# Performance work log

Hardware: AMD Instinct MI355X
Metric: run time of the kernel (lower is better)

## Reference

```python
import jax, jax.numpy as jnp
import numpy as np

L, B, S, D, H = 4, 4, 2048, 512, 8
DH = D // H
FF = 4 * D
BN_EPS = 1e-3  # keras BatchNormalization default epsilon


def setup_inputs() -> dict:
    key = jax.random.key(0)
    ks = jax.random.split(key, 8)
    g = lambda k, shape: jax.random.normal(k, shape, dtype=jnp.float32) * 0.02
    return {
        "sequence": jax.random.normal(ks[0], (B, S, D), dtype=jnp.float32),
        "wq": g(ks[1], (L, D, D)), "bq": jnp.zeros((L, D), jnp.float32),
        "wk": g(ks[2], (L, D, D)), "bk": jnp.zeros((L, D), jnp.float32),
        "wv": g(ks[3], (L, D, D)), "bv": jnp.zeros((L, D), jnp.float32),
        "wo": g(ks[4], (L, D, D)), "bo": jnp.zeros((L, D), jnp.float32),
        "w1": g(ks[5], (L, D, FF)), "b1": jnp.zeros((L, FF), jnp.float32),
        "w2": g(ks[6], (L, FF, D)), "b2": jnp.zeros((L, D), jnp.float32),
        "g1": jnp.ones((L, D), jnp.float32), "be1": jnp.zeros((L, D), jnp.float32),
        "g2": jnp.ones((L, D), jnp.float32), "be2": jnp.zeros((L, D), jnp.float32),
    }


def reference(sequence, wq, bq, wk, bk, wv, bv, wo, bo, w1, b1, w2, b2, g1, be1, g2, be2):
    # Inference-mode BatchNorm with moving_mean=0, moving_var=1:
    # bn(x) = x / sqrt(1 + eps) * gamma + beta
    bn_inv = 1.0 / jnp.sqrt(jnp.float32(1.0 + BN_EPS))
    scale = 1.0 / jnp.sqrt(jnp.float32(DH))
    x = sequence  # [B, S, D]
    for i in range(L):
        # Batched multi-head self-attention (== the per-position loop concat)
        q = (x @ wq[i] + bq[i]).reshape(B, S, H, DH)
        k = (x @ wk[i] + bk[i]).reshape(B, S, H, DH)
        v = (x @ wv[i] + bv[i]).reshape(B, S, H, DH)
        att = jax.nn.softmax(jnp.einsum('bqhd,bkhd->bhqk', q, k) * scale, axis=-1)
        o = jnp.einsum('bhqk,bkhd->bqhd', att, v).reshape(B, S, D)
        o = o @ wo[i] + bo[i]
        x = (x + o) * bn_inv * g1[i] + be1[i]          # residual + BN
        f = jax.nn.relu(x @ w1[i] + b1[i]) @ w2[i] + b2[i]  # FFN
        x = (x + f) * bn_inv * g2[i] + be2[i]          # residual + BN
    return x
```

## Files before the change

kernel.cpp:

```cpp
#include <hip/hip_runtime.h>
#include <hip/hip_bf16.h>

#define BB   4
#define SS   2048
#define DDIM 512
#define HH   8
#define DHD  64
#define FFD  2048
#define LLN  4
#define NQKV 1536
#define BN_INV 0.9995003747f
#define QSCALE 0.18033688011112042f

typedef __bf16 bf16x8 __attribute__((ext_vector_type(8)));
typedef __bf16 bf16x4 __attribute__((ext_vector_type(4)));
typedef float  f32x4  __attribute__((ext_vector_type(4)));
typedef float  f32x16 __attribute__((ext_vector_type(16)));

__device__ __forceinline__ void gl2lds16(const void* g, void* l) {
  __builtin_amdgcn_global_load_lds((const __attribute__((address_space(1))) void*)g,
                                   (__attribute__((address_space(3))) void*)l, 16, 0, 0);
}

__device__ __forceinline__ unsigned pkbf16(float a, float b) {
  union { __bf16 h[2]; unsigned u; } x;
  x.h[0] = (__bf16)a; x.h[1] = (__bf16)b;
  return x.u;
}

__global__ __launch_bounds__(256) void k_transpose_w(const float* __restrict__ in,
                                                     __bf16* __restrict__ out,
                                                     int R, int C,
                                                     size_t in_zs, size_t out_zs) {
  __shared__ float tile[32][33];
  in += (size_t)blockIdx.z * in_zs;
  out += (size_t)blockIdx.z * out_zs;
  const int c0 = blockIdx.x * 32, r0 = blockIdx.y * 32;
  const int tx = threadIdx.x & 31, ty = threadIdx.x >> 5;
#pragma unroll
  for (int k = 0; k < 4; ++k) {
    int r = ty + k * 8;
    tile[r][tx] = in[(size_t)(r0 + r) * C + (c0 + tx)];
  }
  __syncthreads();
#pragma unroll
  for (int k = 0; k < 4; ++k) {
    int c = ty + k * 8;
    out[(size_t)(c0 + c) * R + (r0 + tx)] = (__bf16)tile[tx][c];
  }
}

__global__ __launch_bounds__(256) void k_bias_fuse(const float* __restrict__ bq,
                                                   const float* __restrict__ bk,
                                                   const float* __restrict__ bv,
                                                   float* __restrict__ out) {
  const int i = blockIdx.x * 256 + threadIdx.x;
  const int l = i / NQKV, j = i - l * NQKV;
  float v = (j < 512) ? bq[l * 512 + j]
          : (j < 1024) ? bk[l * 512 + j - 512]
                       : bv[l * 512 + j - 1024];
  out[i] = v;
}

__global__ __launch_bounds__(256) void k_transpose_v(const __bf16* __restrict__ qkv,
                                                     __bf16* __restrict__ vt) {
  __shared__ __bf16 tile[32][33];
  const int s0 = blockIdx.x * 32;
  const int d0 = blockIdx.y * 32;
  const int bh = blockIdx.z, b = bh >> 3, h = bh & 7;
  const int tx = threadIdx.x & 31, ty = threadIdx.x >> 5;
#pragma unroll
  for (int k = 0; k < 4; ++k) {
    int s = ty + k * 8;
    tile[s][tx] = qkv[(size_t)(b * SS + s0 + s) * NQKV + 2 * DDIM + h * DHD + d0 + tx];
  }
  __syncthreads();
#pragma unroll
  for (int k = 0; k < 4; ++k) {
    int d = ty + k * 8;
    vt[(size_t)(bh * DHD + d0 + d) * SS + (s0 + tx)] = tile[tx][d];
  }
}

__global__ __launch_bounds__(256) void k_cast(const float* __restrict__ in,
                                              float* __restrict__ xf,
                                              __bf16* __restrict__ xb) {
  const int i = (blockIdx.x * 256 + threadIdx.x) * 4;
  const float4 v = *(const float4*)(in + i);
  *(float4*)(xf + i) = v;
  bf16x4 o;
  o[0] = (__bf16)v.x; o[1] = (__bf16)v.y; o[2] = (__bf16)v.z; o[3] = (__bf16)v.w;
  *(bf16x4*)(xb + i) = o;
}

template <int EPI>
__global__ __launch_bounds__(256) void k_gemm_bt(const __bf16* __restrict__ A,
                                                 const __bf16* __restrict__ Bt,
                                                 const float* __restrict__ bias,
                                                 __bf16* __restrict__ Cb,
                                                 int M, int N, int K,
                                                 const float* __restrict__ xres,
                                                 float* __restrict__ xout,
                                                 const float* __restrict__ gvec,
                                                 const float* __restrict__ bvec) {
  __shared__ char As[2][16384];
  __shared__ char Bs[2][16384];
  const int tid = threadIdx.x;
  const int l = tid & 63, w = tid >> 6;
  const int wm = w >> 1, wn = w & 1;
  const int m0 = blockIdx.y * 128, n0 = blockIdx.x * 128;
  const int lr = l & 15, lg = l >> 4;
  f32x4 acc[4][4] = {};
  const int nk = K >> 6;
  const size_t ldab = (size_t)K * 2;

  auto stage = [&](int buf, int kt) {
    const int k0b = kt * 128;
#pragma unroll
    for (int i = 0; i < 4; ++i) {
      const int chunk = i * 256 + tid;
      const int row = chunk >> 3;
      const int scb = ((chunk & 7) * 16) ^ ((row & 7) << 4);
      gl2lds16((const char*)A + (size_t)(m0 + row) * ldab + k0b + scb,
               As[buf] + (i * 256 + w * 64) * 16);
      gl2lds16((const char*)Bt + (size_t)(n0 + row) * ldab + k0b + scb,
               Bs[buf] + (i * 256 + w * 64) * 16);
    }
  };

  stage(0, 0);
  __syncthreads();
  int cur = 0;
  for (int kt = 0; kt < nk; ++kt) {
    if (kt + 1 < nk) stage(cur ^ 1, kt + 1);
#pragma unroll
    for (int kk = 0; kk < 2; ++kk) {
      bf16x8 a[4], b[4];
#pragma unroll
      for (int m = 0; m < 4; ++m) {
        const int row = wm * 64 + m * 16 + lr;
        const int cb = kk * 64 + lg * 16;
        a[m] = *(const bf16x8*)(As[cur] + row * 128 + (cb ^ ((row & 7) << 4)));
      }
#pragma unroll
      for (int n = 0; n < 4; ++n) {
        const int row = wn * 64 + n * 16 + lr;
        const int cb = kk * 64 + lg * 16;
        b[n] = *(const bf16x8*)(Bs[cur] + row * 128 + (cb ^ ((row & 7) << 4)));
      }
#pragma unroll
      for (int m = 0; m < 4; ++m)
#pragma unroll
        for (int n = 0; n < 4; ++n)
          acc[m][n] = __builtin_amdgcn_mfma_f32_16x16x32_bf16(a[m], b[n], acc[m][n], 0, 0, 0);
    }
    asm volatile("s_waitcnt vmcnt(0)" ::: "memory");
    __syncthreads();
    cur ^= 1;
  }
#pragma unroll
  for (int m = 0; m < 4; ++m) {
    const int gm = m0 + wm * 64 + m * 16 + lg * 4;
#pragma unroll
    for (int n = 0; n < 4; ++n) {
      const int gn = n0 + wn * 64 + n * 16 + lr;
      const float bv_ = bias[gn];
#pragma unroll
      for (int j = 0; j < 4; ++j) {
        const size_t idx = (size_t)(gm + j) * N + gn;
        float v = acc[m][n][j] + bv_;
        if constexpr (EPI == 1) {
          Cb[idx] = (__bf16)fmaxf(v, 0.0f);
        } else if constexpr (EPI == 2) {
          float t = (xres[idx] + v) * BN_INV * gvec[gn] + bvec[gn];
          xout[idx] = t;
          Cb[idx] = (__bf16)t;
        } else {
          if (gn < DDIM) v *= QSCALE;
          Cb[idx] = (__bf16)v;
        }
      }
    }
  }
}

__global__ __launch_bounds__(256, 2) void k_attn(const __bf16* __restrict__ QKV,
                                                 const __bf16* __restrict__ Vt,
                                                 __bf16* __restrict__ O) {
  __shared__ char smem[65536];
  const int tid = threadIdx.x, l = tid & 63, w = tid >> 6;
  const int lq = l & 31, hi = l >> 5;
  const int f = blockIdx.y * 16 + blockIdx.x;
  const int L = (f & 7) * 64 + (f >> 3);
  const int qt = L & 15, bh = L >> 4;
  const int b = bh >> 3, h = bh & 7;
  const int myq = qt * 128 + w * 32 + lq;
  bf16x8 qf[4];
  {
    const __bf16* qp = QKV + (size_t)(b * SS + myq) * NQKV + h * DHD + hi * 8;
#pragma unroll
    for (int kc = 0; kc < 4; ++kc)
      qf[kc] = *(const bf16x8*)(qp + kc * 16);
  }
  f32x16 oaccT[2] = {};
  float rsum = 0.f;

  auto stage = [&](int buf, int t) {
    const int kv0 = t * 128;
    char* Kd = smem + buf * 16384;
    char* Vd = smem + 32768 + buf * 16384;
#pragma unroll
    for (int i = 0; i < 4; ++i) {
      const int chunk = i * 256 + tid;
      const int row = chunk >> 3;
      const int rs = row ^ ((((row >> 2) + 1) & 2) * 6);
      const int scb = ((chunk & 7) * 16) ^ ((row & 7) << 4);
      gl2lds16((const char*)QKV + ((size_t)(b * SS + kv0 + rs) * NQKV + DDIM + h * DHD) * 2 + scb,
               Kd + (i * 256 + w * 64) * 16);
    }
#pragma unroll
    for (int i = 0; i < 4; ++i) {
      const int chunk = i * 256 + tid;
      const int row = chunk >> 4;
      const int scb = ((chunk & 15) * 16) ^ ((row & 15) << 4);
      gl2lds16((const char*)Vt + ((size_t)(bh * DHD + row) * SS + kv0) * 2 + scb,
               Vd + (i * 256 + w * 64) * 16);
    }
  };

  stage(0, 0);
  __syncthreads();
  int cur = 0;
  for (int t = 0; t < SS / 128; ++t) {
    if (t < SS / 128 - 1) stage(cur ^ 1, t + 1);
    const char* Ks = smem + cur * 16384;
    const char* Vs = smem + 32768 + cur * 16384;
#pragma unroll
    for (int kt2 = 0; kt2 < 4; ++kt2) {
      const int krow = kt2 * 32 + lq;
      const int kswz = (krow & 7) << 4;
      f32x16 st = {};
      __builtin_amdgcn_s_setprio(1);
#pragma unroll
      for (int kc = 0; kc < 4; ++kc) {
        bf16x8 kf = *(const bf16x8*)(Ks + krow * 128 + ((kc * 32 + hi * 16) ^ kswz));
        st = __builtin_amdgcn_mfma_f32_32x32x16_bf16(kf, qf[kc], st, 0, 0, 0);
      }
      __builtin_amdgcn_s_setprio(0);
      unsigned pk8[8];
#pragma unroll
      for (int i = 0; i < 8; ++i) {
        const float e0 = __builtin_amdgcn_exp2f(st[2 * i]);
        const float e1 = __builtin_amdgcn_exp2f(st[2 * i + 1]);
        rsum += e0 + e1;
        pk8[i] = pkbf16(e0, e1);
      }
      union { unsigned u[4]; bf16x8 v; } pf0, pf1;
#pragma unroll
      for (int i = 0; i < 4; ++i) { pf0.u[i] = pk8[i]; pf1.u[i] = pk8[4 + i]; }
      __builtin_amdgcn_s_setprio(1);
#pragma unroll
      for (int dt = 0; dt < 2; ++dt) {
        const int vrow = dt * 32 + lq;
        const int vswz = (vrow & 15) << 4;
        bf16x8 vf0 = *(const bf16x8*)(Vs + vrow * 256 + ((kt2 * 64 + hi * 16) ^ vswz));
        bf16x8 vf1 = *(const bf16x8*)(Vs + vrow * 256 + ((kt2 * 64 + 32 + hi * 16) ^ vswz));
        oaccT[dt] = __builtin_amdgcn_mfma_f32_32x32x16_bf16(vf0, pf0.v, oaccT[dt], 0, 0, 0);
        oaccT[dt] = __builtin_amdgcn_mfma_f32_32x32x16_bf16(vf1, pf1.v, oaccT[dt], 0, 0, 0);
      }
      __builtin_amdgcn_s_setprio(0);
    }
    asm volatile("s_waitcnt vmcnt(0)" ::: "memory");
    __syncthreads();
    cur ^= 1;
  }
  rsum += __shfl_xor(rsum, 32);
  const float inv = 1.0f / rsum;
  __bf16* op = O + (size_t)(b * SS + myq) * DDIM + h * DHD;
#pragma unroll
  for (int dt = 0; dt < 2; ++dt)
#pragma unroll
    for (int g = 0; g < 4; ++g) {
      const int d0 = dt * 32 + g * 8 + hi * 4;
      unsigned u0 = pkbf16(oaccT[dt][4 * g + 0] * inv, oaccT[dt][4 * g + 1] * inv);
      unsigned u1 = pkbf16(oaccT[dt][4 * g + 2] * inv, oaccT[dt][4 * g + 3] * inv);
      uint2 uu; uu.x = u0; uu.y = u1;
      *(uint2*)(op + d0) = uu;
    }
}

static constexpr size_t SZ_WQKVT = (size_t)LLN * NQKV * DDIM * 2;
static constexpr size_t SZ_WOT   = (size_t)LLN * DDIM * DDIM * 2;
static constexpr size_t SZ_WT_DF = (size_t)LLN * DDIM * FFD * 2;
static constexpr size_t SZ_BQKV  = (size_t)LLN * NQKV * 4;
static constexpr size_t SZ_X     = (size_t)BB * SS * DDIM * 4;
static constexpr size_t SZ_ABF   = (size_t)BB * SS * DDIM * 2;
static constexpr size_t SZ_QKV   = (size_t)BB * SS * NQKV * 2;
static constexpr size_t OFF_WQKVT = 0;
static constexpr size_t OFF_WOT  = OFF_WQKVT + SZ_WQKVT;
static constexpr size_t OFF_W1T  = OFF_WOT + SZ_WOT;
static constexpr size_t OFF_W2T  = OFF_W1T + SZ_WT_DF;
static constexpr size_t OFF_BQKV = OFF_W2T + SZ_WT_DF;
static constexpr size_t OFF_X    = OFF_BQKV + SZ_BQKV;
static constexpr size_t OFF_XB   = OFF_X + SZ_X;
static constexpr size_t OFF_QKV  = OFF_XB + SZ_ABF;
static constexpr size_t OFF_VT   = OFF_QKV + SZ_QKV;
static constexpr size_t OFF_OB   = OFF_VT + SZ_ABF;
static constexpr size_t OFF_H1   = OFF_QKV;

extern "C" void kernel_launch(void* const* d_in, const int* in_sizes, int n_in,
                              void* d_out, int out_size, void* d_ws, size_t ws_size,
                              hipStream_t stream) {
  const float* seq = (const float*)d_in[0];
  const float* wq = (const float*)d_in[1];  const float* bq = (const float*)d_in[2];
  const float* wk = (const float*)d_in[3];  const float* bk = (const float*)d_in[4];
  const float* wv = (const float*)d_in[5];  const float* bv = (const float*)d_in[6];
  const float* wo = (const float*)d_in[7];  const float* bo = (const float*)d_in[8];
  const float* w1 = (const float*)d_in[9];  const float* b1 = (const float*)d_in[10];
  const float* w2 = (const float*)d_in[11]; const float* b2 = (const float*)d_in[12];
  const float* g1 = (const float*)d_in[13]; const float* be1 = (const float*)d_in[14];
  const float* g2 = (const float*)d_in[15]; const float* be2 = (const float*)d_in[16];

  char* ws = (char*)d_ws;
  __bf16* wqkvt = (__bf16*)(ws + OFF_WQKVT);
  __bf16* wot = (__bf16*)(ws + OFF_WOT);
  __bf16* w1t = (__bf16*)(ws + OFF_W1T);
  __bf16* w2t = (__bf16*)(ws + OFF_W2T);
  float*  bqkv = (float*)(ws + OFF_BQKV);
  float*  xf  = (float*)(ws + OFF_X);
  __bf16* xb  = (__bf16*)(ws + OFF_XB);
  __bf16* qkvb = (__bf16*)(ws + OFF_QKV);
  __bf16* vtb = (__bf16*)(ws + OFF_VT);
  __bf16* ob  = (__bf16*)(ws + OFF_OB);
  __bf16* h1  = (__bf16*)(ws + OFF_H1);

  const size_t zDD = (size_t)DDIM * DDIM;
  const size_t zQKV = (size_t)NQKV * DDIM;
  const size_t zDF = (size_t)DDIM * FFD;
  k_transpose_w<<<dim3(16, 16, LLN), 256, 0, stream>>>(wq, wqkvt, DDIM, DDIM, zDD, zQKV);
  k_transpose_w<<<dim3(16, 16, LLN), 256, 0, stream>>>(wk, wqkvt + (size_t)DDIM * DDIM, DDIM, DDIM, zDD, zQKV);
  k_transpose_w<<<dim3(16, 16, LLN), 256, 0, stream>>>(wv, wqkvt + (size_t)2 * DDIM * DDIM, DDIM, DDIM, zDD, zQKV);
  k_transpose_w<<<dim3(16, 16, LLN), 256, 0, stream>>>(wo, wot, DDIM, DDIM, zDD, zDD);
  k_transpose_w<<<dim3(64, 16, LLN), 256, 0, stream>>>(w1, w1t, DDIM, FFD, zDF, zDF);
  k_transpose_w<<<dim3(16, 64, LLN), 256, 0, stream>>>(w2, w2t, FFD, DDIM, zDF, zDF);
  k_bias_fuse<<<LLN * NQKV / 256, 256, 0, stream>>>(bq, bk, bv, bqkv);
  k_cast<<<4096, 256, 0, stream>>>(seq, xf, xb);

  const int M = BB * SS;
  for (int i = 0; i < LLN; ++i) {
    k_gemm_bt<3><<<dim3(NQKV / 128, M / 128), 256, 0, stream>>>(
        xb, wqkvt + (size_t)i * NQKV * DDIM, bqkv + i * NQKV, qkvb, M, NQKV, DDIM,
        nullptr, nullptr, nullptr, nullptr);
    k_transpose_v<<<dim3(SS / 32, DHD / 32, BB * HH), 256, 0, stream>>>(qkvb, vtb);
    k_attn<<<dim3(SS / 128, BB * HH), 256, 0, stream>>>(qkvb, vtb, ob);
    k_gemm_bt<2><<<dim3(DDIM / 128, M / 128), 256, 0, stream>>>(
        ob, wot + (size_t)i * DDIM * DDIM, bo + i * DDIM, xb, M, DDIM, DDIM,
        xf, xf, g1 + i * DDIM, be1 + i * DDIM);
    k_gemm_bt<1><<<dim3(FFD / 128, M / 128), 256, 0, stream>>>(
        xb, w1t + (size_t)i * DDIM * FFD, b1 + i * FFD, h1, M, FFD, DDIM,
        nullptr, nullptr, nullptr, nullptr);
    k_gemm_bt<2><<<dim3(DDIM / 128, M / 128), 256, 0, stream>>>(
        h1, w2t + (size_t)i * DDIM * FFD, b2 + i * DDIM, xb, M, DDIM, FFD,
        xf, (i == LLN - 1) ? (float*)d_out : xf, g2 + i * DDIM, be2 + i * DDIM);
  }
  (void)in_sizes; (void)n_in; (void)out_size; (void)ws_size;
}
```

Before: 642.5 us.

## Add 256x256-tile 8-wave GEMM with interleaved prefetch for QKV and FFN1

Adds a new GEMM kernel that uses 256x256 output tiles and 512 threads (8 waves, each computing 128x64). It splits the per-k-tile work into four MFMA phases, with LDS fragment loads and the next tile's global-to-LDS prefetch interleaved between them, and raises wave priority around the MFMA blocks. The QKV projection and the first FFN GEMM now use this kernel to increase data reuse per block and overlap loads with compute. The trade-off is fewer blocks (grids of 6x32 and 8x32), 128KB of LDS per block giving one block per CU, and more barriers per k-step.

```diff
diff --git a/kernel.cpp b/kernel.cpp
--- a/kernel.cpp
+++ b/kernel.cpp
@@ -28,6 +28,8 @@
   return x.u;
 }
 
+#define SBAR() do { __builtin_amdgcn_s_barrier(); asm volatile("" ::: "memory"); } while (0)
+
 __global__ __launch_bounds__(256) void k_transpose_w(const float* __restrict__ in,
                                                      __bf16* __restrict__ out,
                                                      int R, int C,
@@ -103,8 +105,8 @@
                                                  float* __restrict__ xout,
                                                  const float* __restrict__ gvec,
                                                  const float* __restrict__ bvec) {
-  __shared__ char As[2][16384];
-  __shared__ char Bs[2][16384];
+  __shared__ __align__(16) char As[2][16384];
+  __shared__ __align__(16) char Bs[2][16384];
   const int tid = threadIdx.x;
   const int l = tid & 63, w = tid >> 6;
   const int wm = w >> 1, wn = w & 1;
@@ -175,6 +177,159 @@
           float t = (xres[idx] + v) * BN_INV * gvec[gn] + bvec[gn];
           xout[idx] = t;
           Cb[idx] = (__bf16)t;
+        } else {
+          if (gn < DDIM) v *= QSCALE;
+          Cb[idx] = (__bf16)v;
+        }
+      }
+    }
+  }
+}
+
+template <int EPI>
+__global__ __launch_bounds__(512, 1) void k_gemm256(const __bf16* __restrict__ A,
+                                                    const __bf16* __restrict__ Bt,
+                                                    const float* __restrict__ bias,
+                                                    __bf16* __restrict__ Cb,
+                                                    int M, int N, int K) {
+  __shared__ __align__(16) char As[2][32768];
+  __shared__ __align__(16) char Bs[2][32768];
+  const int tid = threadIdx.x;
+  const int l = tid & 63, w = tid >> 6;
+  const int wm = w >> 2, wn = w & 3;
+  const int m0 = blockIdx.y * 256, n0 = blockIdx.x * 256;
+  const int lr = l & 15, lg = l >> 4;
+  f32x4 acc[8][4] = {};
+  const int nk = K >> 6;
+  const size_t ldab = (size_t)K * 2;
+
+  auto stA = [&](int buf, int kt, int h) {
+    const int k0b = kt * 128;
+#pragma unroll
+    for (int i = 0; i < 2; ++i) {
+      const int chunk = h * 1024 + i * 512 + tid;
+      const int row = chunk >> 3;
+      const int scb = ((chunk & 7) * 16) ^ ((row & 7) << 4);
+      gl2lds16((const char*)A + (size_t)(m0 + row) * ldab + k0b + scb,
+               As[buf] + (h * 1024 + i * 512 + w * 64) * 16);
+    }
+  };
+  auto stB = [&](int buf, int kt, int h) {
+    const int k0b = kt * 128;
+#pragma unroll
+    for (int i = 0; i < 2; ++i) {
+      const int chunk = h * 1024 + i * 512 + tid;
+      const int row = chunk >> 3;
+      const int scb = ((chunk & 7) * 16) ^ ((row & 7) << 4);
+      gl2lds16((const char*)Bt + (size_t)(n0 + row) * ldab + k0b + scb,
+               Bs[buf] + (h * 1024 + i * 512 + w * 64) * 16);
+    }
+  };
+
+  stA(0, 0, 0); stA(0, 0, 1); stB(0, 0, 0); stB(0, 0, 1);
+  asm volatile("s_waitcnt vmcnt(0)" ::: "memory");
+  SBAR();
+
+  int cur = 0;
+  for (int kt = 0; kt < nk; ++kt) {
+    const char* Ac = As[cur];
+    const char* Bc = Bs[cur];
+    const int oth = cur ^ 1;
+    const bool pf = (kt + 1 < nk);
+    bf16x8 af[4][2], bfr[4][2];
+#pragma unroll
+    for (int mi = 0; mi < 4; ++mi) {
+      const int row = wm * 128 + mi * 16 + lr;
+      const int swz = (row & 7) << 4;
+#pragma unroll
+      for (int kk = 0; kk < 2; ++kk)
+        af[mi][kk] = *(const bf16x8*)(Ac + row * 128 + ((kk * 64 + lg * 16) ^ swz));
+    }
+#pragma unroll
+    for (int ni = 0; ni < 2; ++ni) {
+      const int row = wn * 64 + ni * 16 + lr;
+      const int swz = (row & 7) << 4;
+#pragma unroll
+      for (int kk = 0; kk < 2; ++kk)
+        bfr[ni][kk] = *(const bf16x8*)(Bc + row * 128 + ((kk * 64 + lg * 16) ^ swz));
+    }
+    if (pf) { stA(oth, kt + 1, 0); stA(oth, kt + 1, 1); }
+    SBAR();
+    __builtin_amdgcn_s_setprio(1);
+#pragma unroll
+    for (int mi = 0; mi < 4; ++mi)
+#pragma unroll
+      for (int ni = 0; ni < 2; ++ni)
+#pragma unroll
+        for (int kk = 0; kk < 2; ++kk)
+          acc[mi][ni] = __builtin_amdgcn_mfma_f32_16x16x32_bf16(af[mi][kk], bfr[ni][kk], acc[mi][ni], 0, 0, 0);
+    __builtin_amdgcn_s_setprio(0);
+    SBAR();
+#pragma unroll
+    for (int ni = 2; ni < 4; ++ni) {
+      const int row = wn * 64 + ni * 16 + lr;
+      const int swz = (row & 7) << 4;
+#pragma unroll
+      for (int kk = 0; kk < 2; ++kk)
+        bfr[ni][kk] = *(const bf16x8*)(Bc + row * 128 + ((kk * 64 + lg * 16) ^ swz));
+    }
+    if (pf) { stB(oth, kt + 1, 0); stB(oth, kt + 1, 1); }
+    SBAR();
+    __builtin_amdgcn_s_setprio(1);
+#pragma unroll
+    for (int mi = 0; mi < 4; ++mi)
+#pragma unroll
+      for (int ni = 2; ni < 4; ++ni)
+#pragma unroll
+        for (int kk = 0; kk < 2; ++kk)
+          acc[mi][ni] = __builtin_amdgcn_mfma_f32_16x16x32_bf16(af[mi][kk], bfr[ni][kk], acc[mi][ni], 0, 0, 0);
+    __builtin_amdgcn_s_setprio(0);
+    SBAR();
+#pragma unroll
+    for (int mi = 0; mi < 4; ++mi) {
+      const int row = wm * 128 + (mi + 4) * 16 + lr;
+      const int swz = (row & 7) << 4;
+#pragma unroll
+      for (int kk = 0; kk < 2; ++kk)
+        af[mi][kk] = *(const bf16x8*)(Ac + row * 128 + ((kk * 64 + lg * 16) ^ swz));
+    }
+    SBAR();
+    __builtin_amdgcn_s_setprio(1);
+#pragma unroll
+    for (int mi = 0; mi < 4; ++mi)
+#pragma unroll
+      for (int ni = 0; ni < 2; ++ni)
+#pragma unroll
+        for (int kk = 0; kk < 2; ++kk)
+          acc[mi + 4][ni] = __builtin_amdgcn_mfma_f32_16x16x32_bf16(af[mi][kk], bfr[ni][kk], acc[mi + 4][ni], 0, 0, 0);
+    __builtin_amdgcn_s_setprio(0);
+    SBAR();
+    __builtin_amdgcn_s_setprio(1);
+#pragma unroll
+    for (int mi = 0; mi < 4; ++mi)
+#pragma unroll
+      for (int ni = 2; ni < 4; ++ni)
+#pragma unroll
+        for (int kk = 0; kk < 2; ++kk)
+          acc[mi + 4][ni] = __builtin_amdgcn_mfma_f32_16x16x32_bf16(af[mi][kk], bfr[ni][kk], acc[mi + 4][ni], 0, 0, 0);
+    __builtin_amdgcn_s_setprio(0);
+    asm volatile("s_waitcnt vmcnt(0)" ::: "memory");
+    SBAR();
+    cur ^= 1;
+  }
+#pragma unroll
+  for (int mi = 0; mi < 8; ++mi) {
+    const int gm = m0 + wm * 128 + mi * 16 + lg * 4;
+#pragma unroll
+    for (int ni = 0; ni < 4; ++ni) {
+      const int gn = n0 + wn * 64 + ni * 16 + lr;
+      const float bv_ = bias[gn];
+#pragma unroll
+      for (int j = 0; j < 4; ++j) {
+        const size_t idx = (size_t)(gm + j) * N + gn;
+        float v = acc[mi][ni][j] + bv_;
+        if constexpr (EPI == 1) {
+          Cb[idx] = (__bf16)fmaxf(v, 0.0f);
         } else {
           if (gn < DDIM) v *= QSCALE;
           Cb[idx] = (__bf16)v;
@@ -348,17 +503,15 @@
 
   const int M = BB * SS;
   for (int i = 0; i < LLN; ++i) {
-    k_gemm_bt<3><<<dim3(NQKV / 128, M / 128), 256, 0, stream>>>(
-        xb, wqkvt + (size_t)i * NQKV * DDIM, bqkv + i * NQKV, qkvb, M, NQKV, DDIM,
-        nullptr, nullptr, nullptr, nullptr);
+    k_gemm256<3><<<dim3(NQKV / 256, M / 256), 512, 0, stream>>>(
+        xb, wqkvt + (size_t)i * NQKV * DDIM, bqkv + i * NQKV, qkvb, M, NQKV, DDIM);
     k_transpose_v<<<dim3(SS / 32, DHD / 32, BB * HH), 256, 0, stream>>>(qkvb, vtb);
     k_attn<<<dim3(SS / 128, BB * HH), 256, 0, stream>>>(qkvb, vtb, ob);
     k_gemm_bt<2><<<dim3(DDIM / 128, M / 128), 256, 0, stream>>>(
         ob, wot + (size_t)i * DDIM * DDIM, bo + i * DDIM, xb, M, DDIM, DDIM,
         xf, xf, g1 + i * DDIM, be1 + i * DDIM);
-    k_gemm_bt<1><<<dim3(FFD / 128, M / 128), 256, 0, stream>>>(
-        xb, w1t + (size_t)i * DDIM * FFD, b1 + i * FFD, h1, M, FFD, DDIM,
-        nullptr, nullptr, nullptr, nullptr);
+    k_gemm256<1><<<dim3(FFD / 256, M / 256), 512, 0, stream>>>(
+        xb, w1t + (size_t)i * DDIM * FFD, b1 + i * FFD, h1, M, FFD, DDIM);
     k_gemm_bt<2><<<dim3(DDIM / 128, M / 128), 256, 0, stream>>>(
         h1, w2t + (size_t)i * DDIM * FFD, b2 + i * DDIM, xb, M, DDIM, FFD,
         xf, (i == LLN - 1) ? (float*)d_out : xf, g2 + i * DDIM, be2 + i * DDIM);
```

New measurement: 641.4 us. Within noise of the previous version (-0.2%).

## Use triple-buffered 512-thread GEMM with partial vmcnt waits and MFMA priority

Applied to the files above, without the earlier changes.

Replaces the double-buffered 256-thread GEMM with a 512-thread version on the same 128x128 tile. Each wave now computes 64x32, and shared-memory staging is triple-buffered, so loads run two k-steps ahead. Each step waits on vmcnt(4) instead of draining all loads and uses one barrier per iteration. s_setprio is raised around the MFMA block. The aim is to hide global-load latency better and to give each CU more waves, at the cost of 96KB of LDS per block (one block per CU) and fewer accumulators per wave.

```diff
diff --git a/kernel.cpp b/kernel.cpp
--- a/kernel.cpp
+++ b/kernel.cpp
@@ -28,6 +28,8 @@
   return x.u;
 }
 
+#define SBAR() do { __builtin_amdgcn_s_barrier(); asm volatile("" ::: "memory"); } while (0)
+
 __global__ __launch_bounds__(256) void k_transpose_w(const float* __restrict__ in,
                                                      __bf16* __restrict__ out,
                                                      int R, int C,
@@ -94,81 +96,95 @@
 }
 
 template <int EPI>
-__global__ __launch_bounds__(256) void k_gemm_bt(const __bf16* __restrict__ A,
-                                                 const __bf16* __restrict__ Bt,
-                                                 const float* __restrict__ bias,
-                                                 __bf16* __restrict__ Cb,
-                                                 int M, int N, int K,
-                                                 const float* __restrict__ xres,
-                                                 float* __restrict__ xout,
-                                                 const float* __restrict__ gvec,
-                                                 const float* __restrict__ bvec) {
-  __shared__ char As[2][16384];
-  __shared__ char Bs[2][16384];
+__global__ __launch_bounds__(512, 1) void k_gemm3(const __bf16* __restrict__ A,
+                                                  const __bf16* __restrict__ Bt,
+                                                  const float* __restrict__ bias,
+                                                  __bf16* __restrict__ Cb,
+                                                  int M, int N, int K,
+                                                  const float* __restrict__ xres,
+                                                  float* __restrict__ xout,
+                                                  const float* __restrict__ gvec,
+                                                  const float* __restrict__ bvec) {
+  __shared__ __align__(16) char As[3][16384];
+  __shared__ __align__(16) char Bs[3][16384];
   const int tid = threadIdx.x;
   const int l = tid & 63, w = tid >> 6;
-  const int wm = w >> 1, wn = w & 1;
+  const int wm = w >> 2, wn = w & 3;
   const int m0 = blockIdx.y * 128, n0 = blockIdx.x * 128;
   const int lr = l & 15, lg = l >> 4;
-  f32x4 acc[4][4] = {};
+  f32x4 acc[4][2] = {};
   const int nk = K >> 6;
   const size_t ldab = (size_t)K * 2;
 
   auto stage = [&](int buf, int kt) {
     const int k0b = kt * 128;
 #pragma unroll
-    for (int i = 0; i < 4; ++i) {
-      const int chunk = i * 256 + tid;
+    for (int i = 0; i < 2; ++i) {
+      const int chunk = i * 512 + tid;
       const int row = chunk >> 3;
       const int scb = ((chunk & 7) * 16) ^ ((row & 7) << 4);
       gl2lds16((const char*)A + (size_t)(m0 + row) * ldab + k0b + scb,
-               As[buf] + (i * 256 + w * 64) * 16);
+               As[buf] + (i * 512 + w * 64) * 16);
       gl2lds16((const char*)Bt + (size_t)(n0 + row) * ldab + k0b + scb,
-               Bs[buf] + (i * 256 + w * 64) * 16);
+               Bs[buf] + (i * 512 + w * 64) * 16);
     }
   };
 
   stage(0, 0);
-  __syncthreads();
-  int cur = 0;
+  stage(1, 1);
+  int bc = 0;
   for (int kt = 0; kt < nk; ++kt) {
-    if (kt + 1 < nk) stage(cur ^ 1, kt + 1);
-#pragma unroll
-    for (int kk = 0; kk < 2; ++kk) {
-      bf16x8 a[4], b[4];
-#pragma unroll
-      for (int m = 0; m < 4; ++m) {
-        const int row = wm * 64 + m * 16 + lr;
-        const int cb = kk * 64 + lg * 16;
-        a[m] = *(const bf16x8*)(As[cur] + row * 128 + (cb ^ ((row & 7) << 4)));
-      }
-#pragma unroll
-      for (int n = 0; n < 4; ++n) {
-        const int row = wn * 64 + n * 16 + lr;
-        const int cb = kk * 64 + lg * 16;
-        b[n] = *(const bf16x8*)(Bs[cur] + row * 128 + (cb ^ ((row & 7) << 4)));
-      }
-#pragma unroll
-      for (int m = 0; m < 4; ++m)
-#pragma unroll
-        for (int n = 0; n < 4; ++n)
-          acc[m][n] = __builtin_amdgcn_mfma_f32_16x16x32_bf16(a[m], b[n], acc[m][n], 0, 0, 0);
-    }
-    asm volatile("s_waitcnt vmcnt(0)" ::: "memory");
-    __syncthreads();
-    cur ^= 1;
-  }
-#pragma unroll
-  for (int m = 0; m < 4; ++m) {
-    const int gm = m0 + wm * 64 + m * 16 + lg * 4;
-#pragma unroll
-    for (int n = 0; n < 4; ++n) {
-      const int gn = n0 + wn * 64 + n * 16 + lr;
+    if (kt + 1 < nk) {
+      asm volatile("s_waitcnt vmcnt(4)" ::: "memory");
+    } else {
+      asm volatile("s_waitcnt vmcnt(0)" ::: "memory");
+    }
+    SBAR();
+    if (kt + 2 < nk) {
+      int bn = bc + 2; if (bn >= 3) bn -= 3;
+      stage(bn, kt + 2);
+    }
+    const char* Ac = As[bc];
+    const char* Bc = Bs[bc];
+    bf16x8 a[4][2], b[2][2];
+#pragma unroll
+    for (int mi = 0; mi < 4; ++mi) {
+      const int row = wm * 64 + mi * 16 + lr;
+      const int swz = (row & 7) << 4;
+#pragma unroll
+      for (int kk = 0; kk < 2; ++kk)
+        a[mi][kk] = *(const bf16x8*)(Ac + row * 128 + ((kk * 64 + lg * 16) ^ swz));
+    }
+#pragma unroll
+    for (int ni = 0; ni < 2; ++ni) {
+      const int row = wn * 32 + ni * 16 + lr;
+      const int swz = (row & 7) << 4;
+#pragma unroll
+      for (int kk = 0; kk < 2; ++kk)
+        b[ni][kk] = *(const bf16x8*)(Bc + row * 128 + ((kk * 64 + lg * 16) ^ swz));
+    }
+    __builtin_amdgcn_s_setprio(1);
+#pragma unroll
+    for (int mi = 0; mi < 4; ++mi)
+#pragma unroll
+      for (int ni = 0; ni < 2; ++ni)
+#pragma unroll
+        for (int kk = 0; kk < 2; ++kk)
+          acc[mi][ni] = __builtin_amdgcn_mfma_f32_16x16x32_bf16(a[mi][kk], b[ni][kk], acc[mi][ni], 0, 0, 0);
+    __builtin_amdgcn_s_setprio(0);
+    if (++bc == 3) bc = 0;
+  }
+#pragma unroll
+  for (int mi = 0; mi < 4; ++mi) {
+    const int gm = m0 + wm * 64 + mi * 16 + lg * 4;
+#pragma unroll
+    for (int ni = 0; ni < 2; ++ni) {
+      const int gn = n0 + wn * 32 + ni * 16 + lr;
       const float bv_ = bias[gn];
 #pragma unroll
       for (int j = 0; j < 4; ++j) {
         const size_t idx = (size_t)(gm + j) * N + gn;
-        float v = acc[m][n][j] + bv_;
+        float v = acc[mi][ni][j] + bv_;
         if constexpr (EPI == 1) {
           Cb[idx] = (__bf16)fmaxf(v, 0.0f);
         } else if constexpr (EPI == 2) {
@@ -348,18 +364,18 @@
 
   const int M = BB * SS;
   for (int i = 0; i < LLN; ++i) {
-    k_gemm_bt<3><<<dim3(NQKV / 128, M / 128), 256, 0, stream>>>(
+    k_gemm3<3><<<dim3(NQKV / 128, M / 128), 512, 0, stream>>>(
         xb, wqkvt + (size_t)i * NQKV * DDIM, bqkv + i * NQKV, qkvb, M, NQKV, DDIM,
         nullptr, nullptr, nullptr, nullptr);
     k_transpose_v<<<dim3(SS / 32, DHD / 32, BB * HH), 256, 0, stream>>>(qkvb, vtb);
     k_attn<<<dim3(SS / 128, BB * HH), 256, 0, stream>>>(qkvb, vtb, ob);
-    k_gemm_bt<2><<<dim3(DDIM / 128, M / 128), 256, 0, stream>>>(
+    k_gemm3<2><<<dim3(DDIM / 128, M / 128), 512, 0, stream>>>(
         ob, wot + (size_t)i * DDIM * DDIM, bo + i * DDIM, xb, M, DDIM, DDIM,
         xf, xf, g1 + i * DDIM, be1 + i * DDIM);
-    k_gemm_bt<1><<<dim3(FFD / 128, M / 128), 256, 0, stream>>>(
+    k_gemm3<1><<<dim3(FFD / 128, M / 128), 512, 0, stream>>>(
         xb, w1t + (size_t)i * DDIM * FFD, b1 + i * FFD, h1, M, FFD, DDIM,
         nullptr, nullptr, nullptr, nullptr);
-    k_gemm_bt<2><<<dim3(DDIM / 128, M / 128), 256, 0, stream>>>(
+    k_gemm3<2><<<dim3(DDIM / 128, M / 128), 512, 0, stream>>>(
         h1, w2t + (size_t)i * DDIM * FFD, b2 + i * DDIM, xb, M, DDIM, FFD,
         xf, (i == LLN - 1) ? (float*)d_out : xf, g2 + i * DDIM, be2 + i * DDIM);
   }
```

Result: slower. 685.0 us (+6.6%).
